# Kernel optimization log

Hardware: AMD Instinct MI355X
Metric: run time of the kernel (lower is better)

Reference implementation:

```python
import jax, jax.numpy as jnp
import numpy as np

N = 256          # fft_size == len(root_sequence)
B = 8            # batch
S = 14           # num_ofdm_symbols
PILOTS = [0, 7]  # pilot OFDM symbol indices
U = 1            # ZC root index


def _gather_index_list():
    # pilot symbols -> 0 (reference shift), data symbols -> 1..num_data
    out, k = [], 1
    for s in range(S):
        if s in PILOTS:
            out.append(0)
        else:
            out.append(k)
            k += 1
    return np.asarray(out, dtype=np.int32)


def setup_inputs() -> dict:
    key = jax.random.key(0)
    ks = jax.random.split(key, 5)
    # Zadoff-Chu root sequence (unit modulus) -> real/imag float32 parts
    n = np.arange(N, dtype=np.float64)
    zc = np.exp(-1j * np.pi * U * n * (n + 1) / N)
    return {
        "x_real": jax.random.normal(ks[0], (B, S, N), dtype=jnp.float32),
        "x_imag": jax.random.normal(ks[1], (B, S, N), dtype=jnp.float32),
        "cov_real": jax.random.normal(ks[2], (N, N, N), dtype=jnp.float32) * 0.05,
        "cov_imag": jax.random.normal(ks[3], (N, N, N), dtype=jnp.float32) * 0.05,
        "zc_real": jnp.asarray(zc.real, dtype=jnp.float32),
        "zc_imag": jnp.asarray(zc.imag, dtype=jnp.float32),
        "shift_val": jax.random.randint(ks[4], (B, S - len(PILOTS)), 0, N, dtype=jnp.int32),
        "gather_idx": jnp.asarray(_gather_index_list()),
    }


def reference(x_real, x_imag, cov_real, cov_imag, zc_real, zc_imag, shift_val, gather_idx):
    x = (x_real + 1j * x_imag).astype(jnp.complex64)            # [B, S, N] received symbols
    cov = (cov_real + 1j * cov_imag).astype(jnp.complex64)      # [N, N, N] LMMSE covariance blocks
    zc = (zc_real + 1j * zc_imag).astype(jnp.complex64)         # [N] root sequence

    # complete_shift_val: prepend reference shift (0), remap via gather_index_list
    complete = jnp.pad(shift_val, ((0, 0), (1, 0)), constant_values=0)  # [B, 1+num_data]
    complete = complete[:, gather_idx]                                   # [B, S]

    # ifft_zc0 = sionna (orthonormal) ifft of the root sequence, shape [1,1,N]
    ifft_zc0 = jnp.fft.ifft(zc, norm="ortho").astype(jnp.complex64)[None, None, :]

    # FFT-based normalized circular cross-correlation along the last axis
    cc = jnp.fft.ifft(jnp.fft.fft(x, axis=-1) * jnp.conj(jnp.fft.fft(ifft_zc0, axis=-1)), axis=-1)
    h_time_est = (cc / jnp.sqrt(jnp.float32(N))).astype(jnp.complex64)   # [B, S, N]

    h_freq_est = jnp.fft.fft(h_time_est, axis=-1).astype(jnp.complex64)  # [B, S, N]

    # LMMSE_TrueP: gather per-shift [N,N] covariance block, apply as mat-vec
    block = cov[complete]                                                # [B, S, N, N]
    h_freq_est = jnp.einsum("bsnm,bsm->bsn", block, h_freq_est)          # [B, S, N]
    return h_freq_est
```

## Files before the change

kernel.cpp:

```cpp
#include <hip/hip_runtime.h>
#include <math.h>

static constexpr int kN   = 256;
static constexpr int kB   = 8;
static constexpr int kS   = 14;
static constexpr int kNSH = 12;
static constexpr int kBS  = kB * kS;

__global__ __launch_bounds__(256) void dft_zc_kernel(
    const float* __restrict__ xr, const float* __restrict__ xi,
    const float* __restrict__ zcr, const float* __restrict__ zci,
    float* __restrict__ hre, float* __restrict__ him)
{
    __shared__ float sxr[kN];
    __shared__ float sxi[kN];
    const int bs = blockIdx.x;
    const int k  = threadIdx.x;

    sxr[k] = xr[bs * kN + k];
    sxi[k] = xi[bs * kN + k];

    const float two_pi_over_N = 6.283185307179586476925f / (float)kN;
    float wi, wr;
    sincosf(-two_pi_over_N * (float)k, &wi, &wr);

    __syncthreads();

    float Hr = 0.0f, Hi = 0.0f;

    for (int n0 = 0; n0 < kN; n0 += 32) {
        const int p = (k * n0) & (kN - 1);
        float ci, cr;
        sincosf(-two_pi_over_N * (float)p, &ci, &cr);
        #pragma unroll
        for (int j = 0; j < 32; ++j) {
            const int n = n0 + j;
            const float a = sxr[n];
            const float b = sxi[n];
            Hr = fmaf(a, cr, fmaf(-b, ci, Hr));
            Hi = fmaf(a, ci, fmaf( b, cr, Hi));
            const float nr = cr * wr - ci * wi;
            const float ni = cr * wi + ci * wr;
            cr = nr; ci = ni;
        }
    }

    const float zr = zcr[k], zi = zci[k];
    hre[bs * kN + k] = fmaf(Hr, zr,  Hi * zi);
    him[bs * kN + k] = fmaf(Hi, zr, -Hr * zi);
}

__global__ __launch_bounds__(256) void matvec_kernel(
    const float* __restrict__ covr, const float* __restrict__ covi,
    const float* __restrict__ hre, const float* __restrict__ him,
    const int*  __restrict__ shift, const int* __restrict__ gidx,
    float* __restrict__ out)
{
    const int bs = blockIdx.x >> 3;
    const int o  = blockIdx.x & 7;
    const int s  = bs % kS;
    const int b  = bs / kS;

    const int g = gidx[s];
    const int c = (g == 0) ? 0 : shift[b * kNSH + (g - 1)];

    const int tid = threadIdx.x;
    const int w   = tid >> 6;
    const int l   = tid & 63;

    const float4 hr = ((const float4*)(hre + bs * kN))[l];
    const float4 hi = ((const float4*)(him + bs * kN))[l];

    const long base = (long)c * (long)(kN * kN);
    const float* __restrict__ rb = covr + base;
    const float* __restrict__ ib = covi + base;
    const int n0 = o * 32 + w * 8;

    float4 mr[8], mi[8];
    #pragma unroll
    for (int r = 0; r < 8; ++r) {
        mr[r] = ((const float4*)(rb + (long)(n0 + r) * kN))[l];
        mi[r] = ((const float4*)(ib + (long)(n0 + r) * kN))[l];
    }

    float ar[8], ai[8];
    #pragma unroll
    for (int r = 0; r < 8; ++r) {
        ar[r] = mr[r].x*hr.x + mr[r].y*hr.y + mr[r].z*hr.z + mr[r].w*hr.w
              - (mi[r].x*hi.x + mi[r].y*hi.y + mi[r].z*hi.z + mi[r].w*hi.w);
        ai[r] = mr[r].x*hi.x + mr[r].y*hi.y + mr[r].z*hi.z + mr[r].w*hi.w
              +  mi[r].x*hr.x + mi[r].y*hr.y + mi[r].z*hr.z + mi[r].w*hr.w;
    }

    #pragma unroll
    for (int off = 32; off > 0; off >>= 1) {
        #pragma unroll
        for (int r = 0; r < 8; ++r) {
            ar[r] += __shfl_xor(ar[r], off, 64);
            ai[r] += __shfl_xor(ai[r], off, 64);
        }
    }

    if (l == 0) {
        #pragma unroll
        for (int r = 0; r < 8; ++r) {
            out[(long)bs * kN + n0 + r]                    = ar[r];
            out[(long)(kBS * kN) + (long)bs * kN + n0 + r] = ai[r];
        }
    }
}

extern "C" void kernel_launch(void* const* d_in, const int* in_sizes, int n_in,
                              void* d_out, int out_size, void* d_ws, size_t ws_size,
                              hipStream_t stream) {
    const float* xr    = (const float*)d_in[0];
    const float* xi    = (const float*)d_in[1];
    const float* covr  = (const float*)d_in[2];
    const float* covi  = (const float*)d_in[3];
    const float* zcr   = (const float*)d_in[4];
    const float* zci   = (const float*)d_in[5];
    const int*   shift = (const int*)d_in[6];
    const int*   gidx  = (const int*)d_in[7];

    float* hre = (float*)d_ws;
    float* him = hre + kBS * kN;

    dft_zc_kernel<<<kBS, 256, 0, stream>>>(xr, xi, zcr, zci, hre, him);
    matvec_kernel<<<kBS * 8, 256, 0, stream>>>(covr, covi, hre, him, shift, gidx,
                                               (float*)d_out);
}
```

Before: 148.1 us.

## Fuse DFT and covariance mat-vec into one kernel, recomputing DFT per block

Merges the DFT/ZC-correlation kernel and the gathered-covariance mat-vec into a single launch. Each of the 8 blocks per (b,s) recomputes the full 256-point DFT in shared memory while its covariance loads are in flight. This removes one kernel launch and the round trip of the intermediate through global memory. The cost is 8x redundant DFT arithmetic and extra register pressure from holding the covariance rows across the DFT loop.

```diff
diff --git a/kernel.cpp b/kernel.cpp
--- a/kernel.cpp
+++ b/kernel.cpp
@@ -7,69 +7,32 @@
 static constexpr int kNSH = 12;
 static constexpr int kBS  = kB * kS;
 
-__global__ __launch_bounds__(256) void dft_zc_kernel(
+__global__ __launch_bounds__(256) void fused_kernel(
     const float* __restrict__ xr, const float* __restrict__ xi,
+    const float* __restrict__ covr, const float* __restrict__ covi,
     const float* __restrict__ zcr, const float* __restrict__ zci,
-    float* __restrict__ hre, float* __restrict__ him)
+    const int*  __restrict__ shift, const int* __restrict__ gidx,
+    float* __restrict__ out)
 {
     __shared__ float sxr[kN];
     __shared__ float sxi[kN];
-    const int bs = blockIdx.x;
-    const int k  = threadIdx.x;
+    __shared__ float shr[kN];
+    __shared__ float shi[kN];
 
-    sxr[k] = xr[bs * kN + k];
-    sxi[k] = xi[bs * kN + k];
-
-    const float two_pi_over_N = 6.283185307179586476925f / (float)kN;
-    float wi, wr;
-    sincosf(-two_pi_over_N * (float)k, &wi, &wr);
-
-    __syncthreads();
-
-    float Hr = 0.0f, Hi = 0.0f;
-
-    for (int n0 = 0; n0 < kN; n0 += 32) {
-        const int p = (k * n0) & (kN - 1);
-        float ci, cr;
-        sincosf(-two_pi_over_N * (float)p, &ci, &cr);
-        #pragma unroll
-        for (int j = 0; j < 32; ++j) {
-            const int n = n0 + j;
-            const float a = sxr[n];
-            const float b = sxi[n];
-            Hr = fmaf(a, cr, fmaf(-b, ci, Hr));
-            Hi = fmaf(a, ci, fmaf( b, cr, Hi));
-            const float nr = cr * wr - ci * wi;
-            const float ni = cr * wi + ci * wr;
-            cr = nr; ci = ni;
-        }
-    }
-
-    const float zr = zcr[k], zi = zci[k];
-    hre[bs * kN + k] = fmaf(Hr, zr,  Hi * zi);
-    him[bs * kN + k] = fmaf(Hi, zr, -Hr * zi);
-}
-
-__global__ __launch_bounds__(256) void matvec_kernel(
-    const float* __restrict__ covr, const float* __restrict__ covi,
-    const float* __restrict__ hre, const float* __restrict__ him,
-    const int*  __restrict__ shift, const int* __restrict__ gidx,
-    float* __restrict__ out)
-{
     const int bs = blockIdx.x >> 3;
     const int o  = blockIdx.x & 7;
     const int s  = bs % kS;
     const int b  = bs / kS;
 
-    const int g = gidx[s];
-    const int c = (g == 0) ? 0 : shift[b * kNSH + (g - 1)];
-
     const int tid = threadIdx.x;
     const int w   = tid >> 6;
     const int l   = tid & 63;
 
-    const float4 hr = ((const float4*)(hre + bs * kN))[l];
-    const float4 hi = ((const float4*)(him + bs * kN))[l];
+    const float xre = xr[bs * kN + tid];
+    const float xim = xi[bs * kN + tid];
+
+    const int g = gidx[s];
+    const int c = (g == 0) ? 0 : shift[b * kNSH + (g - 1)];
 
     const long base = (long)c * (long)(kN * kN);
     const float* __restrict__ rb = covr + base;
@@ -82,6 +45,41 @@
         mr[r] = ((const float4*)(rb + (long)(n0 + r) * kN))[l];
         mi[r] = ((const float4*)(ib + (long)(n0 + r) * kN))[l];
     }
+
+    sxr[tid] = xre;
+    sxi[tid] = xim;
+
+    const float two_pi_over_N = 6.283185307179586476925f / (float)kN;
+    float wi_, wr_;
+    sincosf(-two_pi_over_N * (float)tid, &wi_, &wr_);
+
+    __syncthreads();
+
+    float Hr = 0.0f, Hi = 0.0f;
+    for (int m0 = 0; m0 < kN; m0 += 32) {
+        const int p = (tid * m0) & (kN - 1);
+        float ci_, cr_;
+        sincosf(-two_pi_over_N * (float)p, &ci_, &cr_);
+        #pragma unroll
+        for (int j = 0; j < 32; ++j) {
+            const int m = m0 + j;
+            const float a  = sxr[m];
+            const float bb = sxi[m];
+            Hr = fmaf(a, cr_, fmaf(-bb, ci_, Hr));
+            Hi = fmaf(a, ci_, fmaf( bb, cr_, Hi));
+            const float nr = cr_ * wr_ - ci_ * wi_;
+            const float ni = cr_ * wi_ + ci_ * wr_;
+            cr_ = nr; ci_ = ni;
+        }
+    }
+
+    const float zr = zcr[tid], zi = zci[tid];
+    shr[tid] = fmaf(Hr, zr,  Hi * zi);
+    shi[tid] = fmaf(Hi, zr, -Hr * zi);
+    __syncthreads();
+
+    const float4 hr = ((const float4*)shr)[l];
+    const float4 hi = ((const float4*)shi)[l];
 
     float ar[8], ai[8];
     #pragma unroll
@@ -122,10 +120,8 @@
     const int*   shift = (const int*)d_in[6];
     const int*   gidx  = (const int*)d_in[7];
 
-    float* hre = (float*)d_ws;
-    float* him = hre + kBS * kN;
+    (void)d_ws; (void)ws_size;
 
-    dft_zc_kernel<<<kBS, 256, 0, stream>>>(xr, xi, zcr, zci, hre, him);
-    matvec_kernel<<<kBS * 8, 256, 0, stream>>>(covr, covi, hre, him, shift, gidx,
-                                               (float*)d_out);
+    fused_kernel<<<kBS * 8, 256, 0, stream>>>(xr, xi, covr, covi, zcr, zci,
+                                              shift, gidx, (float*)d_out);
 }
```

New measurement: 149.9 us. Within noise of the previous version (+1.2%).
